# Kernel optimization log

Hardware: AMD Instinct MI355X
Metric: run time of the kernel (lower is better)

Reference implementation:

```python
import jax, jax.numpy as jnp
import numpy as np

TEMPERATURE = 4.0

def setup_inputs() -> dict:
    key = jax.random.key(0)
    k1, k2 = jax.random.split(key)
    query = jax.random.normal(k1, (128, 128, 256), dtype=jnp.float32)      # (B, D, Q)
    context = jax.random.normal(k2, (128, 128, 32, 32), dtype=jnp.float32)  # (B, D, H, W)
    return {"query": query, "context": context}

def reference(query, context):
    B, D, Q = query.shape
    H, W = context.shape[2], context.shape[3]
    L = H * W  # context_length
    context_flat = context.reshape(B, D, L)                    # (B, D, L)
    # scores[b, l, q] = sum_d context[b, d, l] * query[b, d, q]
    scores = jnp.einsum('bdl,bdq->blq', context_flat, query)   # (B, L, Q)
    # first softmax: over query dim (context -> query)
    attn_q = jax.nn.softmax(scores, axis=-1)                   # (B, L, Q)
    # second softmax: over context dim with temperature (query -> context)
    attn_c = jax.nn.softmax(attn_q.transpose(0, 2, 1) * TEMPERATURE, axis=-1)  # (B, Q, L)
    # weighted_context[b, d, q] = sum_l context[b, d, l] * attn_c[b, q, l]
    weighted_context = jnp.einsum('bdl,bql->bdq', context_flat, attn_c)  # (B, D, Q)
    attention_map = attn_c.reshape(B, Q, H, W)
    return (weighted_context, attention_map)
```

## Files before the change

### kernel.cpp

```cpp
#include <hip/hip_runtime.h>
#include <math.h>

#define B_ 128
#define D_ 128
#define Q_ 256
#define L_ 1024

typedef __attribute__((ext_vector_type(8))) short s16x8;
typedef __attribute__((ext_vector_type(4))) float f32x4;
typedef unsigned short u16;

__device__ __forceinline__ u16 f2bf(float x) {
  unsigned u = __float_as_uint(x);
  u += 0x7FFF + ((u >> 16) & 1);
  return (u16)(u >> 16);
}
__device__ __forceinline__ float bf2f(u16 h) {
  return __uint_as_float(((unsigned)h) << 16);
}
__device__ __forceinline__ uint2 pack4bf(float4 v) {
  uint2 r;
  r.x = ((unsigned)f2bf(v.y) << 16) | (unsigned)f2bf(v.x);
  r.y = ((unsigned)f2bf(v.w) << 16) | (unsigned)f2bf(v.z);
  return r;
}
__device__ __forceinline__ void split8(const float* x, s16x8& hi, s16x8& lo) {
#pragma unroll
  for (int j = 0; j < 8; j++) {
    u16 h = f2bf(x[j]);
    hi[j] = (short)h;
    lo[j] = (short)f2bf(x[j] - bf2f(h));
  }
}

__global__ __launch_bounds__(256, 2) void k1_stats(
    const float* __restrict__ query, const float* __restrict__ ctx,
    float* __restrict__ pd, float* __restrict__ fmg, float* __restrict__ fsg) {
  __shared__ float sm[4][64], ss[4][64], fm[64], fs[64];
  const int p = blockIdx.x;
  const int xcd = p & 7, s = p >> 3;
  const int b = xcd + 8 * (s >> 4);
  const int lt = s & 15;
  const int l0 = lt * 64;
  const int tid = threadIdx.x;
  const int wq = tid >> 6;
  const int lane = tid & 63, quad = lane >> 4, l15 = lane & 15;

  const float* Qb = query + (size_t)b * D_ * Q_;
  const float* Cb = ctx + (size_t)b * D_ * L_ + l0;

  f32x4 acc[4][4];
#pragma unroll
  for (int mi = 0; mi < 4; mi++)
#pragma unroll
    for (int ni = 0; ni < 4; ni++) acc[mi][ni] = (f32x4){0.f, 0.f, 0.f, 0.f};

#pragma unroll 2
  for (int k0 = 0; k0 < D_; k0 += 32) {
    const int kq = k0 + quad * 8;
    s16x8 ah[4], al[4], bh[4], bl[4];
#pragma unroll
    for (int mi = 0; mi < 4; mi++) {
      const float* p2 = Qb + (size_t)kq * Q_ + wq * 64 + mi * 16 + l15;
      float x[8];
#pragma unroll
      for (int j = 0; j < 8; j++) x[j] = p2[(size_t)j * Q_];
      split8(x, ah[mi], al[mi]);
    }
#pragma unroll
    for (int ni = 0; ni < 4; ni++) {
      const float* p2 = Cb + (size_t)kq * L_ + ni * 16 + l15;
      float x[8];
#pragma unroll
      for (int j = 0; j < 8; j++) x[j] = p2[(size_t)j * L_];
      split8(x, bh[ni], bl[ni]);
    }
#pragma unroll
    for (int mi = 0; mi < 4; mi++)
#pragma unroll
      for (int ni = 0; ni < 4; ni++) {
        acc[mi][ni] = __builtin_amdgcn_mfma_f32_16x16x32_bf16(
            ah[mi], bh[ni], acc[mi][ni], 0, 0, 0);
        acc[mi][ni] = __builtin_amdgcn_mfma_f32_16x16x32_bf16(
            ah[mi], bl[ni], acc[mi][ni], 0, 0, 0);
        acc[mi][ni] = __builtin_amdgcn_mfma_f32_16x16x32_bf16(
            al[mi], bh[ni], acc[mi][ni], 0, 0, 0);
      }
  }

#pragma unroll
  for (int ni = 0; ni < 4; ni++) {
    float m = -1e30f;
#pragma unroll
    for (int mi = 0; mi < 4; mi++)
#pragma unroll
      for (int r = 0; r < 4; r++) m = fmaxf(m, acc[mi][ni][r]);
    m = fmaxf(m, __shfl_xor(m, 16));
    m = fmaxf(m, __shfl_xor(m, 32));
    float sv = 0.f;
#pragma unroll
    for (int mi = 0; mi < 4; mi++)
#pragma unroll
      for (int r = 0; r < 4; r++) sv += __expf(acc[mi][ni][r] - m);
    sv += __shfl_xor(sv, 16);
    sv += __shfl_xor(sv, 32);
    if (quad == 0) {
      sm[wq][ni * 16 + l15] = m;
      ss[wq][ni * 16 + l15] = sv;
    }
  }
  __syncthreads();
  if (tid < 64) {
    float m0 = sm[0][tid], m1 = sm[1][tid], m2 = sm[2][tid], m3 = sm[3][tid];
    float M = fmaxf(fmaxf(m0, m1), fmaxf(m2, m3));
    float S = ss[0][tid] * __expf(m0 - M) + ss[1][tid] * __expf(m1 - M) +
              ss[2][tid] * __expf(m2 - M) + ss[3][tid] * __expf(m3 - M);
    fm[tid] = M;
    fs[tid] = 1.f / S;
    fmg[(size_t)b * L_ + l0 + tid] = M;
    fsg[(size_t)b * L_ + l0 + tid] = 1.f / S;
  }
  __syncthreads();

  float fmv[4], fiv[4];
#pragma unroll
  for (int ni = 0; ni < 4; ni++) {
    fmv[ni] = fm[ni * 16 + l15];
    fiv[ni] = fs[ni * 16 + l15];
  }
  float dsum[4][4];
#pragma unroll
  for (int mi = 0; mi < 4; mi++)
#pragma unroll
    for (int r = 0; r < 4; r++) dsum[mi][r] = 0.f;
#pragma unroll
  for (int mi = 0; mi < 4; mi++)
#pragma unroll
    for (int r = 0; r < 4; r++) {
#pragma unroll
      for (int ni = 0; ni < 4; ni++) {
        float a = __expf(acc[mi][ni][r] - fmv[ni]) * fiv[ni];
        dsum[mi][r] += __expf(4.f * a);
      }
    }
#pragma unroll
  for (int mi = 0; mi < 4; mi++)
#pragma unroll
    for (int r = 0; r < 4; r++) {
      float v = dsum[mi][r];
      v += __shfl_xor(v, 1);
      v += __shfl_xor(v, 2);
      v += __shfl_xor(v, 4);
      v += __shfl_xor(v, 8);
      dsum[mi][r] = v;
    }
  if (l15 == 0) {
#pragma unroll
    for (int mi = 0; mi < 4; mi++)
#pragma unroll
      for (int r = 0; r < 4; r++)
        pd[(size_t)lt * (B_ * Q_) + b * Q_ + wq * 64 + mi * 16 + quad * 4 +
           r] = dsum[mi][r];
  }
}

__global__ __launch_bounds__(256, 2) void k3_fused(
    const float* __restrict__ query, const float* __restrict__ ctx,
    const float* __restrict__ pd, const float* __restrict__ fmg,
    const float* __restrict__ fsg, float* __restrict__ attn,
    float* __restrict__ W) {
  __shared__ u16 QsH[64][136], QsL[64][136];
  __shared__ u16 As[128][72];
  __shared__ u16 Bs[64][72];
  __shared__ float ivs[64];
  const int p = blockIdx.x;
  const int xcd = p & 7, s = p >> 3;
  const int b = xcd + 8 * (s >> 2);
  const int q0 = (s & 3) * 64;
  const int tid = threadIdx.x;
  const int w = tid >> 6, lane = tid & 63, quad = lane >> 4, l15 = lane & 15;

  if (tid < 64) {
    float sv = 0.f;
#pragma unroll
    for (int t = 0; t < 16; t++)
      sv += pd[(size_t)t * (B_ * Q_) + b * Q_ + q0 + tid];
    ivs[tid] = 1.f / sv;
  }
  {
    const int dr = tid >> 1;
    const int qc = (tid & 1) * 32;
    const float* qp = query + ((size_t)b * D_ + dr) * Q_ + q0 + qc;
#pragma unroll
    for (int c = 0; c < 8; c++) {
      float4 v = *(const float4*)(qp + c * 4);
      float xs[4] = {v.x, v.y, v.z, v.w};
#pragma unroll
      for (int j = 0; j < 4; j++) {
        u16 h = f2bf(xs[j]);
        QsH[qc + c * 4 + j][dr] = h;
        QsL[qc + c * 4 + j][dr] = f2bf(xs[j] - bf2f(h));
      }
    }
  }
  __syncthreads();

  float ivq[4];
#pragma unroll
  for (int ni = 0; ni < 4; ni++) ivq[ni] = ivs[ni * 16 + l15];
  const int wd = (w >> 1) * 64, wn = (w & 1) * 32;
  f32x4 accw[4][2];
#pragma unroll
  for (int mi = 0; mi < 4; mi++)
#pragma unroll
    for (int ni = 0; ni < 2; ni++) accw[mi][ni] = (f32x4){0.f, 0.f, 0.f, 0.f};

  const float* Cb = ctx + (size_t)b * D_ * L_;
  float* Mapb = attn + ((size_t)b * Q_ + q0) * L_;
  const float* fmb = fmg + (size_t)b * L_;
  const float* fsb = fsg + (size_t)b * L_;
  const int dd = tid >> 3;
  const int lc8 = (tid & 7) * 8;

  for (int l0 = 0; l0 < L_; l0 += 64) {
    if (l0) __syncthreads();
#pragma unroll
    for (int h = 0; h < 4; h++) {
      const int d = dd + h * 32;
      const float* cp = Cb + (size_t)d * L_ + l0 + lc8;
      float4 v0 = *(const float4*)cp;
      float4 v1 = *(const float4*)(cp + 4);
      *(uint2*)&As[d][lc8] = pack4bf(v0);
      *(uint2*)&As[d][lc8 + 4] = pack4bf(v1);
    }

    f32x4 accs[4];
#pragma unroll
    for (int ni = 0; ni < 4; ni++) accs[ni] = (f32x4){0.f, 0.f, 0.f, 0.f};
#pragma unroll
    for (int ks = 0; ks < 4; ks++) {
      const float* ap =
          Cb + (size_t)(ks * 32 + quad * 8) * L_ + l0 + 16 * w + l15;
      float x[8];
#pragma unroll
      for (int j = 0; j < 8; j++) x[j] = ap[(size_t)j * L_];
      s16x8 ch, cl;
      split8(x, ch, cl);
#pragma unroll
      for (int ni = 0; ni < 4; ni++) {
        const s16x8 qh = *(const s16x8*)&QsH[ni * 16 + l15][ks * 32 + quad * 8];
        const s16x8 ql = *(const s16x8*)&QsL[ni * 16 + l15][ks * 32 + quad * 8];
        accs[ni] =
            __builtin_amdgcn_mfma_f32_16x16x32_bf16(ch, qh, accs[ni], 0, 0, 0);
        accs[ni] =
            __builtin_amdgcn_mfma_f32_16x16x32_bf16(ch, ql, accs[ni], 0, 0, 0);
        accs[ni] =
            __builtin_amdgcn_mfma_f32_16x16x32_bf16(cl, qh, accs[ni], 0, 0, 0);
      }
    }

    float fml[4], fsl[4];
#pragma unroll
    for (int r = 0; r < 4; r++) {
      fml[r] = fmb[l0 + 16 * w + quad * 4 + r];
      fsl[r] = fsb[l0 + 16 * w + quad * 4 + r];
    }
#pragma unroll
    for (int ni = 0; ni < 4; ni++)
#pragma unroll
      for (int r = 0; r < 4; r++) {
        float a = __expf(accs[ni][r] - fml[r]) * fsl[r];
        float t = __expf(4.f * a) * ivq[ni];
        Mapb[(size_t)(ni * 16 + l15) * L_ + l0 + 16 * w + quad * 4 + r] = t;
        Bs[ni * 16 + l15][16 * w + quad * 4 + r] = f2bf(t);
      }
    __syncthreads();

#pragma unroll
    for (int ks2 = 0; ks2 < 2; ks2++) {
      s16x8 af[4], bq[2];
#pragma unroll
      for (int mi = 0; mi < 4; mi++)
        af[mi] = *(const s16x8*)&As[wd + mi * 16 + l15][ks2 * 32 + quad * 8];
#pragma unroll
      for (int ni = 0; ni < 2; ni++)
        bq[ni] = *(const s16x8*)&Bs[wn + ni * 16 + l15][ks2 * 32 + quad * 8];
#pragma unroll
      for (int mi = 0; mi < 4; mi++)
#pragma unroll
        for (int ni = 0; ni < 2; ni++)
          accw[mi][ni] = __builtin_amdgcn_mfma_f32_16x16x32_bf16(
              af[mi], bq[ni], accw[mi][ni], 0, 0, 0);
    }
  }

  float* Wb = W + (size_t)b * D_ * Q_;
#pragma unroll
  for (int mi = 0; mi < 4; mi++)
#pragma unroll
    for (int ni = 0; ni < 2; ni++)
#pragma unroll
      for (int r = 0; r < 4; r++)
        Wb[(size_t)(wd + mi * 16 + quad * 4 + r) * Q_ + q0 + wn + ni * 16 +
           l15] = accw[mi][ni][r];
}

__global__ __launch_bounds__(256, 2) void k1_attnq_legacy(
    const float* __restrict__ query, const float* __restrict__ ctx,
    float* __restrict__ attq, float* __restrict__ pd) {
  __shared__ float sm[4][64], ss[4][64], fm[64], fs[64];
  const int lt = blockIdx.x, b = blockIdx.y;
  const int l0 = lt * 64;
  const int tid = threadIdx.x;
  const int wq = tid >> 6;
  const int lane = tid & 63, quad = lane >> 4, l15 = lane & 15;

  const float* Qb = query + (size_t)b * D_ * Q_;
  const float* Cb = ctx + (size_t)b * D_ * L_ + l0;

  f32x4 acc[4][4];
#pragma unroll
  for (int mi = 0; mi < 4; mi++)
#pragma unroll
    for (int ni = 0; ni < 4; ni++) acc[mi][ni] = (f32x4){0.f, 0.f, 0.f, 0.f};

#pragma unroll 2
  for (int k0 = 0; k0 < D_; k0 += 32) {
    const int kq = k0 + quad * 8;
    s16x8 ah[4], al[4], bh[4], bl[4];
#pragma unroll
    for (int mi = 0; mi < 4; mi++) {
      const float* p = Qb + (size_t)kq * Q_ + wq * 64 + mi * 16 + l15;
      float x[8];
#pragma unroll
      for (int j = 0; j < 8; j++) x[j] = p[(size_t)j * Q_];
      split8(x, ah[mi], al[mi]);
    }
#pragma unroll
    for (int ni = 0; ni < 4; ni++) {
      const float* p = Cb + (size_t)kq * L_ + ni * 16 + l15;
      float x[8];
#pragma unroll
      for (int j = 0; j < 8; j++) x[j] = p[(size_t)j * L_];
      split8(x, bh[ni], bl[ni]);
    }
#pragma unroll
    for (int mi = 0; mi < 4; mi++)
#pragma unroll
      for (int ni = 0; ni < 4; ni++) {
        acc[mi][ni] = __builtin_amdgcn_mfma_f32_16x16x32_bf16(
            ah[mi], bh[ni], acc[mi][ni], 0, 0, 0);
        acc[mi][ni] = __builtin_amdgcn_mfma_f32_16x16x32_bf16(
            ah[mi], bl[ni], acc[mi][ni], 0, 0, 0);
        acc[mi][ni] = __builtin_amdgcn_mfma_f32_16x16x32_bf16(
            al[mi], bh[ni], acc[mi][ni], 0, 0, 0);
      }
  }

#pragma unroll
  for (int ni = 0; ni < 4; ni++) {
    float m = -1e30f;
#pragma unroll
    for (int mi = 0; mi < 4; mi++)
#pragma unroll
      for (int r = 0; r < 4; r++) m = fmaxf(m, acc[mi][ni][r]);
    m = fmaxf(m, __shfl_xor(m, 16));
    m = fmaxf(m, __shfl_xor(m, 32));
    float s = 0.f;
#pragma unroll
    for (int mi = 0; mi < 4; mi++)
#pragma unroll
      for (int r = 0; r < 4; r++) s += __expf(acc[mi][ni][r] - m);
    s += __shfl_xor(s, 16);
    s += __shfl_xor(s, 32);
    if (quad == 0) {
      sm[wq][ni * 16 + l15] = m;
      ss[wq][ni * 16 + l15] = s;
    }
  }
  __syncthreads();
  if (tid < 64) {
    float m0 = sm[0][tid], m1 = sm[1][tid], m2 = sm[2][tid], m3 = sm[3][tid];
    float M = fmaxf(fmaxf(m0, m1), fmaxf(m2, m3));
    float S = ss[0][tid] * __expf(m0 - M) + ss[1][tid] * __expf(m1 - M) +
              ss[2][tid] * __expf(m2 - M) + ss[3][tid] * __expf(m3 - M);
    fm[tid] = M;
    fs[tid] = 1.f / S;
  }
  __syncthreads();

  float fmv[4], fiv[4];
#pragma unroll
  for (int ni = 0; ni < 4; ni++) {
    fmv[ni] = fm[ni * 16 + l15];
    fiv[ni] = fs[ni * 16 + l15];
  }
  float* Ab = attq + ((size_t)b * Q_ + wq * 64) * L_ + l0;
  float dsum[4][4];
#pragma unroll
  for (int mi = 0; mi < 4; mi++)
#pragma unroll
    for (int r = 0; r < 4; r++) dsum[mi][r] = 0.f;
#pragma unroll
  for (int mi = 0; mi < 4; mi++)
#pragma unroll
    for (int r = 0; r < 4; r++) {
      const int q = mi * 16 + quad * 4 + r;
#pragma unroll
      for (int ni = 0; ni < 4; ni++) {
        float a = __expf(acc[mi][ni][r] - fmv[ni]) * fiv[ni];
        Ab[(size_t)q * L_ + ni * 16 + l15] = a;
        dsum[mi][r] += __expf(4.f * a);
      }
    }
#pragma unroll
  for (int mi = 0; mi < 4; mi++)
#pragma unroll
    for (int r = 0; r < 4; r++) {
      float v = dsum[mi][r];
      v += __shfl_xor(v, 1);
      v += __shfl_xor(v, 2);
      v += __shfl_xor(v, 4);
      v += __shfl_xor(v, 8);
      dsum[mi][r] = v;
    }
  if (l15 == 0) {
#pragma unroll
    for (int mi = 0; mi < 4; mi++)
#pragma unroll
      for (int r = 0; r < 4; r++)
        pd[(size_t)lt * (B_ * Q_) + b * Q_ + wq * 64 + mi * 16 + quad * 4 +
           r] = dsum[mi][r];
  }
}

__global__ __launch_bounds__(256) void k2_invd(const float* __restrict__ pd,
                                               float* __restrict__ invd) {
  const int i = blockIdx.x * 256 + threadIdx.x;
  float s = 0.f;
#pragma unroll
  for (int t = 0; t < 16; t++) s += pd[(size_t)t * (B_ * Q_) + i];
  invd[i] = 1.f / s;
}

__global__ __launch_bounds__(256) void k4_weighted(
    const float* __restrict__ ctx, float* __restrict__ attn,
    const float* __restrict__ invd, float* __restrict__ W) {
  __shared__ unsigned short As[128][32];
  __shared__ unsigned short Bs[64][32];
  const int b = blockIdx.y, q0 = blockIdx.x * 64;
  const int tid = threadIdx.x;
  const int w = tid >> 6, lane = tid & 63, quad = lane >> 4, l15 = lane & 15;
  const int wd = (w >> 1) * 64, wn = (w & 1) * 32;

  const float* Cb = ctx + (size_t)b * D_ * L_;
  float* Ab = attn + ((size_t)b * Q_ + q0) * L_;

  const int lc = (tid & 7) * 4;
  const int rr = tid >> 3;
  const float id0 = invd[b * Q_ + q0 + rr];
  const float id1 = invd[b * Q_ + q0 + rr + 32];

  f32x4 acc[4][2];
#pragma unroll
  for (int mi = 0; mi < 4; mi++)
#pragma unroll
    for (int ni = 0; ni < 2; ni++) acc[mi][ni] = (f32x4){0.f, 0.f, 0.f, 0.f};

  for (int l0 = 0; l0 < L_; l0 += 32) {
    if (l0) __syncthreads();
#pragma unroll
    for (int h = 0; h < 4; h++) {
      const int d = rr + h * 32;
      float4 cv = *(const float4*)(Cb + (size_t)d * L_ + l0 + lc);
      *(uint2*)&As[d][lc] = pack4bf(cv);
    }
#pragma unroll
    for (int h = 0; h < 2; h++) {
      const int q = rr + h * 32;
      float* p = Ab + (size_t)q * L_ + l0 + lc;
      float4 a = *(const float4*)p;
      const float idv = h ? id1 : id0;
      float4 t;
      t.x = __expf(4.f * a.x) * idv;
      t.y = __expf(4.f * a.y) * idv;
      t.z = __expf(4.f * a.z) * idv;
      t.w = __expf(4.f * a.w) * idv;
      *(float4*)p = t;
      *(uint2*)&Bs[q][lc] = pack4bf(t);
    }
    __syncthreads();

    s16x8 af[4], bq[2];
#pragma unroll
    for (int mi = 0; mi < 4; mi++)
      af[mi] = *(const s16x8*)&As[wd + mi * 16 + l15][quad * 8];
#pragma unroll
    for (int ni = 0; ni < 2; ni++)
      bq[ni] = *(const s16x8*)&Bs[wn + ni * 16 + l15][quad * 8];
#pragma unroll
    for (int mi = 0; mi < 4; mi++)
#pragma unroll
      for (int ni = 0; ni < 2; ni++)
        acc[mi][ni] = __builtin_amdgcn_mfma_f32_16x16x32_bf16(
            af[mi], bq[ni], acc[mi][ni], 0, 0, 0);
  }

  float* Wb = W + (size_t)b * D_ * Q_;
#pragma unroll
  for (int mi = 0; mi < 4; mi++)
#pragma unroll
    for (int ni = 0; ni < 2; ni++)
#pragma unroll
      for (int r = 0; r < 4; r++)
        Wb[(size_t)(wd + mi * 16 + quad * 4 + r) * Q_ + q0 + wn + ni * 16 +
           l15] = acc[mi][ni][r];
}

extern "C" void kernel_launch(void* const* d_in, const int* in_sizes, int n_in,
                              void* d_out, int out_size, void* d_ws,
                              size_t ws_size, hipStream_t stream) {
  (void)in_sizes;
  (void)n_in;
  (void)out_size;
  const float* query = (const float*)d_in[0];
  const float* ctx = (const float*)d_in[1];
  float* W = (float*)d_out;
  float* attn = (float*)d_out + (size_t)B_ * D_ * Q_;

  const size_t need =
      ((size_t)16 * B_ * Q_ + (size_t)2 * B_ * L_) * sizeof(float);
  if (d_ws && ws_size >= need) {
    float* pd = (float*)d_ws;
    float* fm = pd + (size_t)16 * B_ * Q_;
    float* fs = fm + (size_t)B_ * L_;
    k1_stats<<<dim3(L_ / 64 * B_), 256, 0, stream>>>(query, ctx, pd, fm, fs);
    k3_fused<<<dim3(Q_ / 64 * B_), 256, 0, stream>>>(query, ctx, pd, fm, fs,
                                                     attn, W);
  } else {
    const size_t need_pd = (size_t)17 * B_ * Q_ * sizeof(float);
    float* pd = (d_ws && ws_size >= need_pd) ? (float*)d_ws : W;
    float* invd = pd + (size_t)16 * B_ * Q_;
    k1_attnq_legacy<<<dim3(L_ / 64, B_), 256, 0, stream>>>(query, ctx, attn,
                                                           pd);
    k2_invd<<<dim3(B_ * Q_ / 256), 256, 0, stream>>>(pd, invd);
    k4_weighted<<<dim3(Q_ / 64, B_), 256, 0, stream>>>(ctx, attn, invd, W);
  }
}
```

Before: 288.1 us.

## Store fp16 attn_q from stats kernel instead of recomputing scores in second pass

The first kernel now writes the normalized first-softmax probabilities as fp16 into workspace, and a new second kernel reads them back instead of recomputing the score GEMM from query and context. This drops the split-bf16 score recomputation (three MFMAs per tile) in the second pass. In exchange it adds about 64MB of fp16 writes and reads, and the second softmax is now computed from fp16-rounded attention values. The new path runs only when the workspace is large enough.

```diff
diff --git a/kernel.cpp b/kernel.cpp
--- a/kernel.cpp
+++ b/kernel.cpp
@@ -17,6 +17,12 @@
 }
 __device__ __forceinline__ float bf2f(u16 h) {
   return __uint_as_float(((unsigned)h) << 16);
+}
+__device__ __forceinline__ u16 f2h(float x) {
+  return __builtin_bit_cast(u16, (_Float16)x);
+}
+__device__ __forceinline__ float h2f(u16 h) {
+  return (float)__builtin_bit_cast(_Float16, h);
 }
 __device__ __forceinline__ uint2 pack4bf(float4 v) {
   uint2 r;
@@ -34,6 +40,261 @@
 }
 
 __global__ __launch_bounds__(256, 2) void k1_stats(
+    const float* __restrict__ query, const float* __restrict__ ctx,
+    float* __restrict__ pd, u16* __restrict__ attq16) {
+  __shared__ float sm[4][64], ss[4][64], fm[64], fs[64];
+  const int p = blockIdx.x;
+  const int xcd = p & 7, s = p >> 3;
+  const int b = xcd + 8 * (s >> 4);
+  const int lt = s & 15;
+  const int l0 = lt * 64;
+  const int tid = threadIdx.x;
+  const int wq = tid >> 6;
+  const int lane = tid & 63, quad = lane >> 4, l15 = lane & 15;
+
+  const float* Qb = query + (size_t)b * D_ * Q_;
+  const float* Cb = ctx + (size_t)b * D_ * L_ + l0;
+
+  f32x4 acc[4][4];
+#pragma unroll
+  for (int mi = 0; mi < 4; mi++)
+#pragma unroll
+    for (int ni = 0; ni < 4; ni++) acc[mi][ni] = (f32x4){0.f, 0.f, 0.f, 0.f};
+
+#pragma unroll 2
+  for (int k0 = 0; k0 < D_; k0 += 32) {
+    const int kq = k0 + quad * 8;
+    s16x8 ah[4], al[4], bh[4], bl[4];
+#pragma unroll
+    for (int mi = 0; mi < 4; mi++) {
+      const float* p2 = Qb + (size_t)kq * Q_ + wq * 64 + mi * 16 + l15;
+      float x[8];
+#pragma unroll
+      for (int j = 0; j < 8; j++) x[j] = p2[(size_t)j * Q_];
+      split8(x, ah[mi], al[mi]);
+    }
+#pragma unroll
+    for (int ni = 0; ni < 4; ni++) {
+      const float* p2 = Cb + (size_t)kq * L_ + ni * 16 + l15;
+      float x[8];
+#pragma unroll
+      for (int j = 0; j < 8; j++) x[j] = p2[(size_t)j * L_];
+      split8(x, bh[ni], bl[ni]);
+    }
+#pragma unroll
+    for (int mi = 0; mi < 4; mi++)
+#pragma unroll
+      for (int ni = 0; ni < 4; ni++) {
+        acc[mi][ni] = __builtin_amdgcn_mfma_f32_16x16x32_bf16(
+            ah[mi], bh[ni], acc[mi][ni], 0, 0, 0);
+        acc[mi][ni] = __builtin_amdgcn_mfma_f32_16x16x32_bf16(
+            ah[mi], bl[ni], acc[mi][ni], 0, 0, 0);
+        acc[mi][ni] = __builtin_amdgcn_mfma_f32_16x16x32_bf16(
+            al[mi], bh[ni], acc[mi][ni], 0, 0, 0);
+      }
+  }
+
+#pragma unroll
+  for (int ni = 0; ni < 4; ni++) {
+    float m = -1e30f;
+#pragma unroll
+    for (int mi = 0; mi < 4; mi++)
+#pragma unroll
+      for (int r = 0; r < 4; r++) m = fmaxf(m, acc[mi][ni][r]);
+    m = fmaxf(m, __shfl_xor(m, 16));
+    m = fmaxf(m, __shfl_xor(m, 32));
+    float sv = 0.f;
+#pragma unroll
+    for (int mi = 0; mi < 4; mi++)
+#pragma unroll
+      for (int r = 0; r < 4; r++) sv += __expf(acc[mi][ni][r] - m);
+    sv += __shfl_xor(sv, 16);
+    sv += __shfl_xor(sv, 32);
+    if (quad == 0) {
+      sm[wq][ni * 16 + l15] = m;
+      ss[wq][ni * 16 + l15] = sv;
+    }
+  }
+  __syncthreads();
+  if (tid < 64) {
+    float m0 = sm[0][tid], m1 = sm[1][tid], m2 = sm[2][tid], m3 = sm[3][tid];
+    float M = fmaxf(fmaxf(m0, m1), fmaxf(m2, m3));
+    float S = ss[0][tid] * __expf(m0 - M) + ss[1][tid] * __expf(m1 - M) +
+              ss[2][tid] * __expf(m2 - M) + ss[3][tid] * __expf(m3 - M);
+    fm[tid] = M;
+    fs[tid] = 1.f / S;
+  }
+  __syncthreads();
+
+  float fmv[4], fiv[4];
+#pragma unroll
+  for (int ni = 0; ni < 4; ni++) {
+    fmv[ni] = fm[ni * 16 + l15];
+    fiv[ni] = fs[ni * 16 + l15];
+  }
+  u16* Ab16 = attq16 + ((size_t)b * Q_ + wq * 64) * L_ + l0;
+  float dsum[4][4];
+#pragma unroll
+  for (int mi = 0; mi < 4; mi++)
+#pragma unroll
+    for (int r = 0; r < 4; r++) dsum[mi][r] = 0.f;
+#pragma unroll
+  for (int mi = 0; mi < 4; mi++)
+#pragma unroll
+    for (int r = 0; r < 4; r++) {
+      const int q = mi * 16 + quad * 4 + r;
+#pragma unroll
+      for (int ni = 0; ni < 4; ni++) {
+        float a = __expf(acc[mi][ni][r] - fmv[ni]) * fiv[ni];
+        u16 ah16 = f2h(a);
+        Ab16[(size_t)q * L_ + ni * 16 + l15] = ah16;
+        dsum[mi][r] += __expf(4.f * h2f(ah16));
+      }
+    }
+#pragma unroll
+  for (int mi = 0; mi < 4; mi++)
+#pragma unroll
+    for (int r = 0; r < 4; r++) {
+      float v = dsum[mi][r];
+      v += __shfl_xor(v, 1);
+      v += __shfl_xor(v, 2);
+      v += __shfl_xor(v, 4);
+      v += __shfl_xor(v, 8);
+      dsum[mi][r] = v;
+    }
+  if (l15 == 0) {
+#pragma unroll
+    for (int mi = 0; mi < 4; mi++)
+#pragma unroll
+      for (int r = 0; r < 4; r++)
+        pd[(size_t)lt * (B_ * Q_) + b * Q_ + wq * 64 + mi * 16 + quad * 4 +
+           r] = dsum[mi][r];
+  }
+}
+
+__global__ __launch_bounds__(256, 2) void k3_direct(
+    const float* __restrict__ ctx, const u16* __restrict__ attq16,
+    const float* __restrict__ pd, float* __restrict__ attn,
+    float* __restrict__ W) {
+  __shared__ u16 As[128][72];
+  __shared__ u16 Bs[64][72];
+  __shared__ float ivs[64];
+  const int p = blockIdx.x;
+  const int xcd = p & 7, s = p >> 3;
+  const int b = xcd + 8 * (s >> 2);
+  const int q0 = (s & 3) * 64;
+  const int tid = threadIdx.x;
+  const int w = tid >> 6, lane = tid & 63, quad = lane >> 4, l15 = lane & 15;
+
+  if (tid < 64) {
+    float sv = 0.f;
+#pragma unroll
+    for (int t = 0; t < 16; t++)
+      sv += pd[(size_t)t * (B_ * Q_) + b * Q_ + q0 + tid];
+    ivs[tid] = 1.f / sv;
+  }
+  __syncthreads();
+
+  const int rr = tid >> 3;
+  const int lc = (tid & 7) * 8;
+  const float id0 = ivs[rr];
+  const float id1 = ivs[rr + 32];
+  const int mq = tid >> 2;
+  const int mc = (tid & 3) * 16;
+
+  const float* Cb = ctx + (size_t)b * D_ * L_;
+  const u16* Aq = attq16 + ((size_t)b * Q_ + q0) * L_;
+  float* Mapb = attn + ((size_t)b * Q_ + q0) * L_;
+
+  const int wd = (w >> 1) * 64, wn = (w & 1) * 32;
+  f32x4 accw[4][2];
+#pragma unroll
+  for (int mi = 0; mi < 4; mi++)
+#pragma unroll
+    for (int ni = 0; ni < 2; ni++) accw[mi][ni] = (f32x4){0.f, 0.f, 0.f, 0.f};
+
+  for (int l0 = 0; l0 < L_; l0 += 64) {
+    if (l0) __syncthreads();
+#pragma unroll
+    for (int h = 0; h < 4; h++) {
+      const int d = rr + h * 32;
+      const float* cp = Cb + (size_t)d * L_ + l0 + lc;
+      float4 v0 = *(const float4*)cp;
+      float4 v1 = *(const float4*)(cp + 4);
+      *(uint2*)&As[d][lc] = pack4bf(v0);
+      *(uint2*)&As[d][lc + 4] = pack4bf(v1);
+    }
+#pragma unroll
+    for (int h = 0; h < 2; h++) {
+      const int q = rr + h * 32;
+      uint4 av = *(const uint4*)(Aq + (size_t)q * L_ + l0 + lc);
+      const float idv = h ? id1 : id0;
+      unsigned wbits[4] = {av.x, av.y, av.z, av.w};
+      unsigned pk[4];
+#pragma unroll
+      for (int c = 0; c < 4; c++) {
+        float a0 = h2f((u16)(wbits[c] & 0xFFFF));
+        float a1 = h2f((u16)(wbits[c] >> 16));
+        float t0 = __expf(4.f * a0) * idv;
+        float t1 = __expf(4.f * a1) * idv;
+        pk[c] = ((unsigned)f2bf(t1) << 16) | (unsigned)f2bf(t0);
+      }
+      *(uint2*)&Bs[q][lc] = make_uint2(pk[0], pk[1]);
+      *(uint2*)&Bs[q][lc + 4] = make_uint2(pk[2], pk[3]);
+    }
+    __syncthreads();
+
+    {
+      const s16x8 m0 = *(const s16x8*)&Bs[mq][mc];
+      const s16x8 m1 = *(const s16x8*)&Bs[mq][mc + 8];
+      float* mp = Mapb + (size_t)mq * L_ + l0 + mc;
+#pragma unroll
+      for (int c = 0; c < 2; c++) {
+        const s16x8& mv = c ? m1 : m0;
+        float4 o0, o1;
+        o0.x = bf2f((u16)mv[0]);
+        o0.y = bf2f((u16)mv[1]);
+        o0.z = bf2f((u16)mv[2]);
+        o0.w = bf2f((u16)mv[3]);
+        o1.x = bf2f((u16)mv[4]);
+        o1.y = bf2f((u16)mv[5]);
+        o1.z = bf2f((u16)mv[6]);
+        o1.w = bf2f((u16)mv[7]);
+        *(float4*)(mp + c * 8) = o0;
+        *(float4*)(mp + c * 8 + 4) = o1;
+      }
+    }
+
+#pragma unroll
+    for (int ks2 = 0; ks2 < 2; ks2++) {
+      s16x8 af[4], bq[2];
+#pragma unroll
+      for (int mi = 0; mi < 4; mi++)
+        af[mi] = *(const s16x8*)&As[wd + mi * 16 + l15][ks2 * 32 + quad * 8];
+#pragma unroll
+      for (int ni = 0; ni < 2; ni++)
+        bq[ni] = *(const s16x8*)&Bs[wn + ni * 16 + l15][ks2 * 32 + quad * 8];
+#pragma unroll
+      for (int mi = 0; mi < 4; mi++)
+#pragma unroll
+        for (int ni = 0; ni < 2; ni++)
+          accw[mi][ni] = __builtin_amdgcn_mfma_f32_16x16x32_bf16(
+              af[mi], bq[ni], accw[mi][ni], 0, 0, 0);
+    }
+  }
+
+  float* Wb = W + (size_t)b * D_ * Q_;
+#pragma unroll
+  for (int mi = 0; mi < 4; mi++)
+#pragma unroll
+    for (int ni = 0; ni < 2; ni++)
+#pragma unroll
+      for (int r = 0; r < 4; r++)
+        Wb[(size_t)(wd + mi * 16 + quad * 4 + r) * Q_ + q0 + wn + ni * 16 +
+           l15] = accw[mi][ni][r];
+}
+
+__global__ __launch_bounds__(256, 2) void k1_statsR6(
     const float* __restrict__ query, const float* __restrict__ ctx,
     float* __restrict__ pd, float* __restrict__ fmg, float* __restrict__ fsg) {
   __shared__ float sm[4][64], ss[4][64], fm[64], fs[64];
@@ -164,7 +425,7 @@
   }
 }
 
-__global__ __launch_bounds__(256, 2) void k3_fused(
+__global__ __launch_bounds__(256, 2) void k3_fusedR6(
     const float* __restrict__ query, const float* __restrict__ ctx,
     const float* __restrict__ pd, const float* __restrict__ fmg,
     const float* __restrict__ fsg, float* __restrict__ attn,
@@ -528,15 +789,24 @@
   float* W = (float*)d_out;
   float* attn = (float*)d_out + (size_t)B_ * D_ * Q_;
 
-  const size_t need =
+  const size_t nAtt = (size_t)B_ * Q_ * L_;
+  const size_t need_full =
+      nAtt * sizeof(u16) + (size_t)16 * B_ * Q_ * sizeof(float);
+  const size_t need_mid =
       ((size_t)16 * B_ * Q_ + (size_t)2 * B_ * L_) * sizeof(float);
-  if (d_ws && ws_size >= need) {
+
+  if (d_ws && ws_size >= need_full) {
+    u16* a16 = (u16*)d_ws;
+    float* pd = (float*)(a16 + nAtt);
+    k1_stats<<<dim3(L_ / 64 * B_), 256, 0, stream>>>(query, ctx, pd, a16);
+    k3_direct<<<dim3(Q_ / 64 * B_), 256, 0, stream>>>(ctx, a16, pd, attn, W);
+  } else if (d_ws && ws_size >= need_mid) {
     float* pd = (float*)d_ws;
     float* fm = pd + (size_t)16 * B_ * Q_;
     float* fs = fm + (size_t)B_ * L_;
-    k1_stats<<<dim3(L_ / 64 * B_), 256, 0, stream>>>(query, ctx, pd, fm, fs);
-    k3_fused<<<dim3(Q_ / 64 * B_), 256, 0, stream>>>(query, ctx, pd, fm, fs,
-                                                     attn, W);
+    k1_statsR6<<<dim3(L_ / 64 * B_), 256, 0, stream>>>(query, ctx, pd, fm, fs);
+    k3_fusedR6<<<dim3(Q_ / 64 * B_), 256, 0, stream>>>(query, ctx, pd, fm, fs,
+                                                       attn, W);
   } else {
     const size_t need_pd = (size_t)17 * B_ * Q_ * sizeof(float);
     float* pd = (d_ws && ws_size >= need_pd) ? (float*)d_ws : W;
```

Result: slower. 298.9 us (+3.7%).
